# Optimization experiments

Measured on AMD Instinct MI355X. Metric: run time of the kernel, lower is better.

Reference implementation:

```python
import jax, jax.numpy as jnp
import numpy as np

EMBED_DIM = 512
NUM_HEADS = 8
HEAD_DIM = EMBED_DIM // NUM_HEADS


def setup_inputs() -> dict:
    key = jax.random.key(0)
    ks = jax.random.split(key, 9)
    s = 1.0 / np.sqrt(EMBED_DIM)
    x = jax.random.normal(ks[0], (2, 4096, EMBED_DIM), dtype=jnp.float32)
    return {
        "x": x,
        "Wq": jax.random.uniform(ks[1], (EMBED_DIM, EMBED_DIM), jnp.float32, -s, s),
        "bq": jax.random.uniform(ks[2], (EMBED_DIM,), jnp.float32, -s, s),
        "Wk": jax.random.uniform(ks[3], (EMBED_DIM, EMBED_DIM), jnp.float32, -s, s),
        "bk": jax.random.uniform(ks[4], (EMBED_DIM,), jnp.float32, -s, s),
        "Wv": jax.random.uniform(ks[5], (EMBED_DIM, EMBED_DIM), jnp.float32, -s, s),
        "bv": jax.random.uniform(ks[6], (EMBED_DIM,), jnp.float32, -s, s),
        "Wo": jax.random.uniform(ks[7], (EMBED_DIM, EMBED_DIM), jnp.float32, -s, s),
        "bo": jax.random.uniform(ks[8], (EMBED_DIM,), jnp.float32, -s, s),
    }


def reference(x, Wq, bq, Wk, bk, Wv, bv, Wo, bo):
    B, S, E = x.shape
    H, D = NUM_HEADS, HEAD_DIM
    # projections (torch Linear: x @ W.T + b)
    q = (x @ Wq.T + bq).reshape(B, S, H, D).transpose(0, 2, 1, 3)  # [B,H,S,D]
    k = (x @ Wk.T + bk).reshape(B, S, H, D).transpose(0, 2, 1, 3)
    v = (x @ Wv.T + bv).reshape(B, S, H, D).transpose(0, 2, 1, 3)
    scores = jnp.einsum("bhsd,bhtd->bhst", q, k) / np.sqrt(D)  # [B,H,S,S]
    attn = jax.nn.softmax(scores, axis=-1)
    out = jnp.einsum("bhst,bhtd->bhsd", attn, v)  # [B,H,S,D]
    out = out.transpose(0, 2, 1, 3).reshape(B, S, E)
    return out @ Wo.T + bo + x
```

## Files before the change

kernel.cpp:

```cpp
#include <hip/hip_runtime.h>
#include <hip/hip_bf16.h>


typedef __attribute__((ext_vector_type(8))) short short8;
typedef __attribute__((ext_vector_type(4))) short short4v;
typedef __attribute__((ext_vector_type(4))) float floatx4;
typedef __attribute__((ext_vector_type(2))) float floatx2;

#define SEQ 4096
#define EMB 512
#define NH 8
#define HD 64
#define MROWS 8192
#define SC2 0.18033688011112042f

__device__ inline unsigned short f2bf_rne(float f) {
    union { float f; unsigned int u; } c; c.f = f;
    unsigned int u = c.u;
    return (unsigned short)((u + 0x7FFFu + ((u >> 16) & 1u)) >> 16);
}

__device__ inline short8 load8f(const float* __restrict__ p) {
    float4 a = *(const float4*)p;
    float4 b = *(const float4*)(p + 4);
    short8 r;
    r[0] = (short)f2bf_rne(a.x); r[1] = (short)f2bf_rne(a.y);
    r[2] = (short)f2bf_rne(a.z); r[3] = (short)f2bf_rne(a.w);
    r[4] = (short)f2bf_rne(b.x); r[5] = (short)f2bf_rne(b.y);
    r[6] = (short)f2bf_rne(b.z); r[7] = (short)f2bf_rne(b.w);
    return r;
}

__device__ inline void gload_lds16(const unsigned short* g, unsigned short* l) {
    __builtin_amdgcn_global_load_lds(
        (__attribute__((address_space(1))) void*)(void*)g,
        (__attribute__((address_space(3))) void*)l,
        16, 0, 0);
}

__device__ inline unsigned int pk_bf2(float a, float b) {
    union { float f; unsigned int u; } ca, cb; ca.f = a; cb.f = b;
    return __builtin_amdgcn_perm(cb.u + 0x8000u, ca.u + 0x8000u, 0x07060302u);
}

__device__ inline unsigned int pk_bf2t(float a, float b) {
    union { float f; unsigned int u; } ca, cb; ca.f = a; cb.f = b;
    return __builtin_amdgcn_perm(cb.u, ca.u, 0x07060302u);
}

__global__ __launch_bounds__(256) void convert_kernel(
    const float* __restrict__ x, const float* __restrict__ Wq,
    const float* __restrict__ Wk, const float* __restrict__ Wv,
    const float* __restrict__ Wo, unsigned short* __restrict__ xb,
    unsigned short* __restrict__ wb)
{
    const size_t i8 = ((size_t)blockIdx.x * 256 + threadIdx.x) * 8;
    const float* src; unsigned short* dst;
    if (i8 < (size_t)MROWS * EMB) { src = x + i8; dst = xb + i8; }
    else {
        size_t j = i8 - (size_t)MROWS * EMB;
        int w = (int)(j >> 18); size_t off = j & 262143;
        src = (w == 0 ? Wq : w == 1 ? Wk : w == 2 ? Wv : Wo) + off;
        dst = wb + (size_t)w * 262144 + off;
    }
    *(short8*)dst = load8f(src);
}

__global__ __launch_bounds__(256) void qkv_kernel(
    const unsigned short* __restrict__ xb, const unsigned short* __restrict__ wb,
    const float* __restrict__ bq, const float* __restrict__ bk,
    const float* __restrict__ bv, unsigned short* __restrict__ Qo,
    unsigned short* __restrict__ Ko, unsigned short* __restrict__ VTo)
{
    __shared__ unsigned short smem[32768];

    const int tid = threadIdx.x, wave = tid >> 6, lane = tid & 63;
    const int quad = lane >> 4, l16 = lane & 15;
    const int wm = wave >> 1, wn = wave & 1;
    const int row0 = blockIdx.x * 128, col0 = blockIdx.y * 128;
    const int z = blockIdx.z;

    unsigned short* sA = smem;
    unsigned short* sB = smem + 16384;

    const unsigned short* A = xb + (size_t)row0 * EMB;
    const unsigned short* Bm = wb + (size_t)z * 262144 + (size_t)col0 * EMB;
    const float* bias = z == 0 ? bq : z == 1 ? bk : bv;
    unsigned short* out = z == 0 ? Qo : z == 1 ? Ko : VTo;

    auto stage = [&](int buf, int k0) {
#pragma unroll
        for (int it = 0; it < 4; ++it) {
            const int s = it * 256 + tid;
            const int row = s >> 3, cg = (s & 7) ^ (row & 7);
            const size_t go = (size_t)row * EMB + k0 + cg * 8;
            gload_lds16(A + go, &sA[buf * 8192 + (it * 256 + wave * 64) * 8]);
            gload_lds16(Bm + go, &sB[buf * 8192 + (it * 256 + wave * 64) * 8]);
        }
    };

    floatx4 acc[4][4];
#pragma unroll
    for (int i = 0; i < 4; ++i)
#pragma unroll
        for (int j = 0; j < 4; ++j) { floatx4 zz = {0.f,0.f,0.f,0.f}; acc[i][j] = zz; }

    stage(0, 0);
    int buf = 0;
    for (int k0 = 0; k0 < EMB; k0 += 64) {
        __syncthreads();
        if (k0 + 64 < EMB) stage(buf ^ 1, k0 + 64);
#pragma unroll
        for (int kk = 0; kk < 2; ++kk) {
            short8 a[4], b[4];
#pragma unroll
            for (int mi = 0; mi < 4; ++mi)
                a[mi] = *(const short8*)&sA[buf * 8192 + (wm * 64 + mi * 16 + l16) * 64 + (((kk * 4 + quad) ^ (l16 & 7)) << 3)];
#pragma unroll
            for (int ni = 0; ni < 4; ++ni)
                b[ni] = *(const short8*)&sB[buf * 8192 + (wn * 64 + ni * 16 + l16) * 64 + (((kk * 4 + quad) ^ (l16 & 7)) << 3)];
            if (z != 2) {
#pragma unroll
                for (int i = 0; i < 4; ++i)
#pragma unroll
                    for (int j = 0; j < 4; ++j)
                        acc[i][j] = __builtin_amdgcn_mfma_f32_16x16x32_bf16(b[i], a[j], acc[i][j], 0, 0, 0);
            } else {
#pragma unroll
                for (int i = 0; i < 4; ++i)
#pragma unroll
                    for (int j = 0; j < 4; ++j)
                        acc[i][j] = __builtin_amdgcn_mfma_f32_16x16x32_bf16(a[i], b[j], acc[i][j], 0, 0, 0);
            }
        }
        buf ^= 1;
    }

    __syncthreads();
    unsigned short* ct = smem;
    const float qs = (z == 0) ? SC2 : 1.0f;
    if (z != 2) {
#pragma unroll
        for (int i = 0; i < 4; ++i) {
            const int n0 = wn * 64 + i * 16 + quad * 4;
            const float4 fb = *(const float4*)&bias[col0 + n0];
#pragma unroll
            for (int j = 0; j < 4; ++j) {
                const int m = wm * 64 + j * 16 + l16;
                ushort4 pk;
                pk.x = f2bf_rne((acc[i][j][0] + fb.x) * qs);
                pk.y = f2bf_rne((acc[i][j][1] + fb.y) * qs);
                pk.z = f2bf_rne((acc[i][j][2] + fb.z) * qs);
                pk.w = f2bf_rne((acc[i][j][3] + fb.w) * qs);
                *(ushort4*)&ct[m * 132 + n0] = pk;
            }
        }
    } else {
#pragma unroll
        for (int j = 0; j < 4; ++j) {
            const int n = wn * 64 + j * 16 + l16;
            const float fb = bias[col0 + n];
#pragma unroll
            for (int i = 0; i < 4; ++i) {
                const int m0 = wm * 64 + i * 16 + quad * 4;
                ushort4 pk;
                pk.x = f2bf_rne(acc[i][j][0] + fb);
                pk.y = f2bf_rne(acc[i][j][1] + fb);
                pk.z = f2bf_rne(acc[i][j][2] + fb);
                pk.w = f2bf_rne(acc[i][j][3] + fb);
                *(ushort4*)&ct[n * 132 + m0] = pk;
            }
        }
    }
    __syncthreads();
#pragma unroll
    for (int it = 0; it < 8; ++it) {
        const int idx = it * 256 + tid;
        const int row = idx >> 4, chunk = idx & 15;
        short8 v = *(const short8*)&ct[row * 132 + chunk * 8];
        size_t addr;
        if (z != 2) {
            const int m_g = row0 + row;
            const int b = m_g >> 12, s = m_g & 4095;
            const int n_g = col0 + chunk * 8;
            const int h = n_g >> 6, d = n_g & 63;
            addr = ((size_t)((b * NH + h) * SEQ + s)) * HD + d;
        } else {
            const int n_g = col0 + row;
            const int h = n_g >> 6, d = n_g & 63;
            const int m_g = row0 + chunk * 8;
            const int b = m_g >> 12, s0 = m_g & 4095;
            addr = ((size_t)((b * NH + h) * HD + d)) * SEQ + s0;
        }
        *(short8*)&out[addr] = v;
    }
}

__global__ __launch_bounds__(512) void attn_kernel(
    const unsigned short* __restrict__ Q, const unsigned short* __restrict__ K,
    const unsigned short* __restrict__ VT, unsigned short* __restrict__ Oout)
{
    __shared__ unsigned short sK[2][2][4096];
    __shared__ unsigned short sVT[2][2][4096];

    const int tid = threadIdx.x, wave = tid >> 6, lane = tid & 63;
    const int quad = lane >> 4, l16 = lane & 15;
    const int bh = blockIdx.x, q0 = blockIdx.y * 128;
    const int xm = l16 & 7;

    const unsigned short* Qh = Q + (size_t)bh * SEQ * HD;
    const unsigned short* Kh = K + (size_t)bh * SEQ * HD;
    const unsigned short* Vh = VT + (size_t)bh * HD * SEQ;

    short8 qf[2];
#pragma unroll
    for (int kk = 0; kk < 2; ++kk)
        qf[kk] = *(const short8*)(Qh + (size_t)(q0 + wave * 16 + l16) * HD + kk * 32 + quad * 8);

    int kbase[4], kx0[4], kx1[4];
#pragma unroll
    for (int nt = 0; nt < 4; ++nt) {
        const int g = nt >> 1, T = nt & 1;
        const int R = g * 32 + ((l16 >> 2) << 3) + (T << 2) + (l16 & 3);
        const int fR = (R & 7) ^ ((R >> 2) & 7);
        kbase[nt] = R * 64;
        kx0[nt] = (quad ^ fR) << 3;
        kx1[nt] = ((4 + quad) ^ fR) << 3;
    }

    floatx4 oacc[4];
#pragma unroll
    for (int dt = 0; dt < 4; ++dt) { floatx4 zz = {0.f,0.f,0.f,0.f}; oacc[dt] = zz; }
    floatx2 psum2 = {0.f, 0.f};
    const floatx4 z4 = {0.f, 0.f, 0.f, 0.f};

    auto stage = [&](int buf, int t0) {
        const int r = tid >> 3, j = tid & 7;
        const int cK = j ^ ((r & 7) ^ ((r >> 2) & 7));
        const int cV = j ^ (r & 7);
#pragma unroll
        for (int sub = 0; sub < 2; ++sub) {
            gload_lds16(Kh + (size_t)(t0 + sub * 64 + r) * HD + cK * 8, &sK[buf][sub][wave * 512]);
            gload_lds16(Vh + (size_t)r * SEQ + t0 + sub * 64 + cV * 8, &sVT[buf][sub][wave * 512]);
        }
    };

    stage(0, 0);
    int buf = 0;
    for (int t0 = 0; t0 < SEQ; t0 += 128) {
        __syncthreads();
        if (t0 + 128 < SEQ) stage(buf ^ 1, t0 + 128);

#pragma unroll
        for (int sub = 0; sub < 2; ++sub) {
            const unsigned short* sKs  = sK[buf][sub];
            const unsigned short* sVTs = sVT[buf][sub];

            floatx4 stf[4];
            {
                short8 bK[4];
#pragma unroll
                for (int nt = 0; nt < 4; ++nt)
                    bK[nt] = *(const short8*)&sKs[kbase[nt] + kx0[nt]];
#pragma unroll
                for (int nt = 0; nt < 4; ++nt)
                    stf[nt] = __builtin_amdgcn_mfma_f32_16x16x32_bf16(bK[nt], qf[0], z4, 0, 0, 0);
            }
            {
                short8 bK[4];
#pragma unroll
                for (int nt = 0; nt < 4; ++nt)
                    bK[nt] = *(const short8*)&sKs[kbase[nt] + kx1[nt]];
#pragma unroll
                for (int nt = 0; nt < 4; ++nt)
                    stf[nt] = __builtin_amdgcn_mfma_f32_16x16x32_bf16(bK[nt], qf[1], stf[nt], 0, 0, 0);
            }

            short8 paf[2];
#pragma unroll
            for (int g = 0; g < 2; ++g) {
                float e[8];
#pragma unroll
                for (int T = 0; T < 2; ++T)
#pragma unroll
                    for (int r = 0; r < 4; ++r)
                        e[T * 4 + r] = __builtin_amdgcn_exp2f(stf[g * 2 + T][r]);
                floatx2 pa = {e[0], e[1]}, pb = {e[2], e[3]};
                floatx2 pc = {e[4], e[5]}, pd = {e[6], e[7]};
                psum2 += (pa + pb) + (pc + pd);
                union { uint4 u; short8 s; } cv;
                cv.u.x = pk_bf2t(e[0], e[1]);
                cv.u.y = pk_bf2t(e[2], e[3]);
                cv.u.z = pk_bf2t(e[4], e[5]);
                cv.u.w = pk_bf2t(e[6], e[7]);
                paf[g] = cv.s;
            }

#pragma unroll
            for (int g = 0; g < 2; ++g) {
                short8 bv8[4];
#pragma unroll
                for (int dt = 0; dt < 4; ++dt)
                    bv8[dt] = *(const short8*)&sVTs[(dt * 16 + l16) * 64 + (((g * 4 + quad) ^ xm) << 3)];
#pragma unroll
                for (int dt = 0; dt < 4; ++dt)
                    oacc[dt] = __builtin_amdgcn_mfma_f32_16x16x32_bf16(paf[g], bv8[dt], oacc[dt], 0, 0, 0);
            }
        }
        buf ^= 1;
    }

    float psum = psum2[0] + psum2[1];
    psum += __shfl_xor(psum, 16);
    psum += __shfl_xor(psum, 32);

    const int b = bh >> 3, h = bh & 7;
#pragma unroll
    for (int r = 0; r < 4; ++r) {
        const float inv = 1.0f / __shfl(psum, quad * 4 + r);
        const int s = q0 + wave * 16 + quad * 4 + r;
        const size_t base = ((size_t)b * SEQ + s) * EMB + h * HD;
#pragma unroll
        for (int dt = 0; dt < 4; ++dt)
            Oout[base + dt * 16 + l16] = f2bf_rne(oacc[dt][r] * inv);
    }
}

__global__ __launch_bounds__(256) void outproj_kernel(
    const unsigned short* __restrict__ Ain, const unsigned short* __restrict__ wob,
    const float* __restrict__ bias, const float* __restrict__ X,
    float* __restrict__ out)
{
    __shared__ unsigned short sA[2][4096];
    __shared__ unsigned short sB[2][8192];

    const int tid = threadIdx.x, wave = tid >> 6, lane = tid & 63;
    const int quad = lane >> 4, l16 = lane & 15;
    const int wm = wave >> 1, wn = wave & 1;
    const int row0 = blockIdx.x * 64, col0 = blockIdx.y * 128;

    const unsigned short* A = Ain + (size_t)row0 * EMB;
    const unsigned short* Bm = wob + (size_t)col0 * EMB;

    auto stage = [&](int buf, int k0) {
#pragma unroll
        for (int it = 0; it < 2; ++it) {
            const int s = it * 256 + tid;
            const int row = s >> 3, cg = (s & 7) ^ (row & 7);
            gload_lds16(A + (size_t)row * EMB + k0 + cg * 8, &sA[buf][(it * 256 + wave * 64) * 8]);
        }
#pragma unroll
        for (int it = 0; it < 4; ++it) {
            const int s = it * 256 + tid;
            const int row = s >> 3, cg = (s & 7) ^ (row & 7);
            gload_lds16(Bm + (size_t)row * EMB + k0 + cg * 8, &sB[buf][(it * 256 + wave * 64) * 8]);
        }
    };

    floatx4 acc[2][4];
#pragma unroll
    for (int mi = 0; mi < 2; ++mi)
#pragma unroll
        for (int ni = 0; ni < 4; ++ni) { floatx4 zz = {0.f,0.f,0.f,0.f}; acc[mi][ni] = zz; }

    stage(0, 0);
    int buf = 0;
    for (int k0 = 0; k0 < EMB; k0 += 64) {
        __syncthreads();
        if (k0 + 64 < EMB) stage(buf ^ 1, k0 + 64);
#pragma unroll
        for (int kk = 0; kk < 2; ++kk) {
            short8 a[2], b[4];
#pragma unroll
            for (int mi = 0; mi < 2; ++mi)
                a[mi] = *(const short8*)&sA[buf][(wm * 32 + mi * 16 + l16) * 64 + (((kk * 4 + quad) ^ (l16 & 7)) << 3)];
#pragma unroll
            for (int ni = 0; ni < 4; ++ni)
                b[ni] = *(const short8*)&sB[buf][(wn * 64 + ni * 16 + l16) * 64 + (((kk * 4 + quad) ^ (l16 & 7)) << 3)];
#pragma unroll
            for (int mi = 0; mi < 2; ++mi)
#pragma unroll
                for (int ni = 0; ni < 4; ++ni)
                    acc[mi][ni] = __builtin_amdgcn_mfma_f32_16x16x32_bf16(a[mi], b[ni], acc[mi][ni], 0, 0, 0);
        }
        buf ^= 1;
    }

#pragma unroll
    for (int mi = 0; mi < 2; ++mi)
#pragma unroll
        for (int ni = 0; ni < 4; ++ni) {
            const int n = col0 + wn * 64 + ni * 16 + l16;
            const float bs = bias[n];
#pragma unroll
            for (int r = 0; r < 4; ++r) {
                const int m = row0 + wm * 32 + mi * 16 + quad * 4 + r;
                const size_t idx = (size_t)m * EMB + n;
                out[idx] = acc[mi][ni][r] + bs + X[idx];
            }
        }
}

extern "C" void kernel_launch(void* const* d_in, const int* in_sizes, int n_in,
                              void* d_out, int out_size, void* d_ws, size_t ws_size,
                              hipStream_t stream) {
    const float* x  = (const float*)d_in[0];
    const float* Wq = (const float*)d_in[1];
    const float* bq = (const float*)d_in[2];
    const float* Wk = (const float*)d_in[3];
    const float* bk = (const float*)d_in[4];
    const float* Wv = (const float*)d_in[5];
    const float* bv = (const float*)d_in[6];
    const float* Wo = (const float*)d_in[7];
    const float* bo = (const float*)d_in[8];
    float* out = (float*)d_out;

    const size_t SZ = (size_t)MROWS * EMB;
    unsigned short* wsXB = (unsigned short*)d_ws;
    unsigned short* wsWB = wsXB + SZ;
    unsigned short* wsQ  = wsWB + 4 * 262144;
    unsigned short* wsK  = wsQ + SZ;
    unsigned short* wsVT = wsK + SZ;

    convert_kernel<<<2560, 256, 0, stream>>>(x, Wq, Wk, Wv, Wo, wsXB, wsWB);
    qkv_kernel<<<dim3(MROWS / 128, EMB / 128, 3), 256, 0, stream>>>(
        wsXB, wsWB, bq, bk, bv, wsQ, wsK, wsVT);
    attn_kernel<<<dim3(2 * NH, SEQ / 128), 512, 0, stream>>>(wsQ, wsK, wsVT, wsXB);
    outproj_kernel<<<dim3(MROWS / 64, EMB / 128), 256, 0, stream>>>(
        wsXB, wsWB + 3 * 262144, bo, x, out);
}
```

Measured before the change: 192.4 us.

## Split attention key dimension across waves with cross-wave output reduction

Reworks the attention kernel so each 256-thread block handles 64 queries and each wave owns a 32-key slice of every 128-key tile while covering all 64 query rows. Partial P·V outputs are then reduced across waves through shared memory. The row sums of exp are now computed with an MFMA against a ones vector instead of VALU adds. This is meant to reuse K/V fragments loaded from LDS across four query sub-tiles and to allow two blocks per CU, at the cost of more accumulator registers and an extra shared-memory reduction at the end.

New measurement: 198.2 us. +3.0%, slower.

```diff
diff --git a/kernel.cpp b/kernel.cpp
--- a/kernel.cpp
+++ b/kernel.cpp
@@ -196,52 +196,63 @@
     }
 }
 
-__global__ __launch_bounds__(512) void attn_kernel(
+__global__ __launch_bounds__(256, 2) void attn_kernel(
     const unsigned short* __restrict__ Q, const unsigned short* __restrict__ K,
     const unsigned short* __restrict__ VT, unsigned short* __restrict__ Oout)
 {
-    __shared__ unsigned short sK[2][2][4096];
-    __shared__ unsigned short sVT[2][2][4096];
+    __shared__ unsigned short smem[32768];
+    __shared__ float sPS[256];
 
     const int tid = threadIdx.x, wave = tid >> 6, lane = tid & 63;
     const int quad = lane >> 4, l16 = lane & 15;
-    const int bh = blockIdx.x, q0 = blockIdx.y * 128;
+    const int bh = blockIdx.x, q0 = blockIdx.y * 64;
     const int xm = l16 & 7;
 
     const unsigned short* Qh = Q + (size_t)bh * SEQ * HD;
     const unsigned short* Kh = K + (size_t)bh * SEQ * HD;
     const unsigned short* Vh = VT + (size_t)bh * HD * SEQ;
 
-    short8 qf[2];
-#pragma unroll
-    for (int kk = 0; kk < 2; ++kk)
-        qf[kk] = *(const short8*)(Qh + (size_t)(q0 + wave * 16 + l16) * HD + kk * 32 + quad * 8);
-
-    int kbase[4], kx0[4], kx1[4];
-#pragma unroll
-    for (int nt = 0; nt < 4; ++nt) {
-        const int g = nt >> 1, T = nt & 1;
-        const int R = g * 32 + ((l16 >> 2) << 3) + (T << 2) + (l16 & 3);
+    short8 qf[4][2];
+#pragma unroll
+    for (int mi = 0; mi < 4; ++mi)
+#pragma unroll
+        for (int kk = 0; kk < 2; ++kk)
+            qf[mi][kk] = *(const short8*)(Qh + (size_t)(q0 + mi * 16 + l16) * HD + kk * 32 + quad * 8);
+
+    int kbase[2], kx0[2], kx1[2];
+#pragma unroll
+    for (int T = 0; T < 2; ++T) {
+        const int R = wave * 32 + ((l16 >> 2) << 3) + (T << 2) + (l16 & 3);
         const int fR = (R & 7) ^ ((R >> 2) & 7);
-        kbase[nt] = R * 64;
-        kx0[nt] = (quad ^ fR) << 3;
-        kx1[nt] = ((4 + quad) ^ fR) << 3;
-    }
-
-    floatx4 oacc[4];
-#pragma unroll
-    for (int dt = 0; dt < 4; ++dt) { floatx4 zz = {0.f,0.f,0.f,0.f}; oacc[dt] = zz; }
-    floatx2 psum2 = {0.f, 0.f};
+        kbase[T] = R * 64;
+        kx0[T] = (quad ^ fR) << 3;
+        kx1[T] = ((4 + quad) ^ fR) << 3;
+    }
+
+    floatx4 oacc[4][4];
+#pragma unroll
+    for (int mi = 0; mi < 4; ++mi)
+#pragma unroll
+        for (int dt = 0; dt < 4; ++dt) { floatx4 zz = {0.f,0.f,0.f,0.f}; oacc[mi][dt] = zz; }
+    floatx4 sacc[4];
+#pragma unroll
+    for (int mi = 0; mi < 4; ++mi) { floatx4 zz = {0.f,0.f,0.f,0.f}; sacc[mi] = zz; }
     const floatx4 z4 = {0.f, 0.f, 0.f, 0.f};
+    const short ob = (short)0x3F80;
+    const short8 ones8 = {ob, ob, ob, ob, ob, ob, ob, ob};
 
     auto stage = [&](int buf, int t0) {
-        const int r = tid >> 3, j = tid & 7;
-        const int cK = j ^ ((r & 7) ^ ((r >> 2) & 7));
-        const int cV = j ^ (r & 7);
-#pragma unroll
-        for (int sub = 0; sub < 2; ++sub) {
-            gload_lds16(Kh + (size_t)(t0 + sub * 64 + r) * HD + cK * 8, &sK[buf][sub][wave * 512]);
-            gload_lds16(Vh + (size_t)r * SEQ + t0 + sub * 64 + cV * 8, &sVT[buf][sub][wave * 512]);
+        unsigned short* sK  = &smem[buf * 16384];
+        unsigned short* sVT = &smem[buf * 16384 + 8192];
+#pragma unroll
+        for (int it = 0; it < 4; ++it) {
+            const int s = it * 256 + tid;
+            const int rK = s >> 3, jK = s & 7;
+            const int cK = jK ^ ((rK & 7) ^ ((rK >> 2) & 7));
+            gload_lds16(Kh + (size_t)(t0 + rK) * HD + cK * 8, &sK[(it * 256 + wave * 64) * 8]);
+            const int rV = s >> 4, jV = s & 15;
+            const int cV = jV ^ (rV & 7);
+            gload_lds16(Vh + (size_t)rV * SEQ + t0 + cV * 8, &sVT[(it * 256 + wave * 64) * 8]);
         }
     };
 
@@ -251,78 +262,93 @@
         __syncthreads();
         if (t0 + 128 < SEQ) stage(buf ^ 1, t0 + 128);
 
-#pragma unroll
-        for (int sub = 0; sub < 2; ++sub) {
-            const unsigned short* sKs  = sK[buf][sub];
-            const unsigned short* sVTs = sVT[buf][sub];
-
-            floatx4 stf[4];
-            {
-                short8 bK[4];
-#pragma unroll
-                for (int nt = 0; nt < 4; ++nt)
-                    bK[nt] = *(const short8*)&sKs[kbase[nt] + kx0[nt]];
-#pragma unroll
-                for (int nt = 0; nt < 4; ++nt)
-                    stf[nt] = __builtin_amdgcn_mfma_f32_16x16x32_bf16(bK[nt], qf[0], z4, 0, 0, 0);
+        const unsigned short* sKs  = &smem[buf * 16384];
+        const unsigned short* sVTs = &smem[buf * 16384 + 8192];
+
+        short8 bK0[2], bK1[2];
+#pragma unroll
+        for (int T = 0; T < 2; ++T) {
+            bK0[T] = *(const short8*)&sKs[kbase[T] + kx0[T]];
+            bK1[T] = *(const short8*)&sKs[kbase[T] + kx1[T]];
+        }
+        short8 bv8[4];
+#pragma unroll
+        for (int dt = 0; dt < 4; ++dt)
+            bv8[dt] = *(const short8*)&sVTs[(dt * 16 + l16) * 128 + (((wave * 4 + quad) ^ xm) << 3)];
+
+#pragma unroll
+        for (int mi = 0; mi < 4; ++mi) {
+            floatx4 s0 = __builtin_amdgcn_mfma_f32_16x16x32_bf16(bK0[0], qf[mi][0], z4, 0, 0, 0);
+            floatx4 s1 = __builtin_amdgcn_mfma_f32_16x16x32_bf16(bK0[1], qf[mi][0], z4, 0, 0, 0);
+            s0 = __builtin_amdgcn_mfma_f32_16x16x32_bf16(bK1[0], qf[mi][1], s0, 0, 0, 0);
+            s1 = __builtin_amdgcn_mfma_f32_16x16x32_bf16(bK1[1], qf[mi][1], s1, 0, 0, 0);
+
+            float e0 = __builtin_amdgcn_exp2f(s0[0]);
+            float e1 = __builtin_amdgcn_exp2f(s0[1]);
+            float e2 = __builtin_amdgcn_exp2f(s0[2]);
+            float e3 = __builtin_amdgcn_exp2f(s0[3]);
+            float e4 = __builtin_amdgcn_exp2f(s1[0]);
+            float e5 = __builtin_amdgcn_exp2f(s1[1]);
+            float e6 = __builtin_amdgcn_exp2f(s1[2]);
+            float e7 = __builtin_amdgcn_exp2f(s1[3]);
+            union { uint4 u; short8 s; } cv;
+            cv.u.x = pk_bf2t(e0, e1);
+            cv.u.y = pk_bf2t(e2, e3);
+            cv.u.z = pk_bf2t(e4, e5);
+            cv.u.w = pk_bf2t(e6, e7);
+            const short8 paf = cv.s;
+
+            sacc[mi] = __builtin_amdgcn_mfma_f32_16x16x32_bf16(paf, ones8, sacc[mi], 0, 0, 0);
+#pragma unroll
+            for (int dt = 0; dt < 4; ++dt)
+                oacc[mi][dt] = __builtin_amdgcn_mfma_f32_16x16x32_bf16(paf, bv8[dt], oacc[mi][dt], 0, 0, 0);
+        }
+        buf ^= 1;
+    }
+
+    if (l16 == 0) {
+#pragma unroll
+        for (int mi = 0; mi < 4; ++mi)
+#pragma unroll
+            for (int r = 0; r < 4; ++r)
+                sPS[wave * 64 + mi * 16 + quad * 4 + r] = sacc[mi][r];
+    }
+
+    float* sRed = (float*)smem;
+    const int b = bh >> 3, h = bh & 7;
+    const int qr = wave * 16 + l16;
+
+#pragma unroll
+    for (int hh = 0; hh < 2; ++hh) {
+        __syncthreads();
+#pragma unroll
+        for (int mi = 0; mi < 4; ++mi)
+#pragma unroll
+            for (int dd = 0; dd < 2; ++dd)
+#pragma unroll
+                for (int r = 0; r < 4; ++r)
+                    sRed[wave * 2176 + (mi * 16 + quad * 4 + r) * 34 + dd * 16 + l16] =
+                        oacc[mi][hh * 2 + dd][r];
+        __syncthreads();
+        floatx2 o8[4] = {{0.f,0.f},{0.f,0.f},{0.f,0.f},{0.f,0.f}};
+#pragma unroll
+        for (int w2 = 0; w2 < 4; ++w2) {
+            const float* base = &sRed[w2 * 2176 + qr * 34 + quad * 8];
+#pragma unroll
+            for (int p = 0; p < 4; ++p) {
+                floatx2 v = *(const floatx2*)(base + p * 2);
+                o8[p] += v;
             }
-            {
-                short8 bK[4];
-#pragma unroll
-                for (int nt = 0; nt < 4; ++nt)
-                    bK[nt] = *(const short8*)&sKs[kbase[nt] + kx1[nt]];
-#pragma unroll
-                for (int nt = 0; nt < 4; ++nt)
-                    stf[nt] = __builtin_amdgcn_mfma_f32_16x16x32_bf16(bK[nt], qf[1], stf[nt], 0, 0, 0);
-            }
-
-            short8 paf[2];
-#pragma unroll
-            for (int g = 0; g < 2; ++g) {
-                float e[8];
-#pragma unroll
-                for (int T = 0; T < 2; ++T)
-#pragma unroll
-                    for (int r = 0; r < 4; ++r)
-                        e[T * 4 + r] = __builtin_amdgcn_exp2f(stf[g * 2 + T][r]);
-                floatx2 pa = {e[0], e[1]}, pb = {e[2], e[3]};
-                floatx2 pc = {e[4], e[5]}, pd = {e[6], e[7]};
-                psum2 += (pa + pb) + (pc + pd);
-                union { uint4 u; short8 s; } cv;
-                cv.u.x = pk_bf2t(e[0], e[1]);
-                cv.u.y = pk_bf2t(e[2], e[3]);
-                cv.u.z = pk_bf2t(e[4], e[5]);
-                cv.u.w = pk_bf2t(e[6], e[7]);
-                paf[g] = cv.s;
-            }
-
-#pragma unroll
-            for (int g = 0; g < 2; ++g) {
-                short8 bv8[4];
-#pragma unroll
-                for (int dt = 0; dt < 4; ++dt)
-                    bv8[dt] = *(const short8*)&sVTs[(dt * 16 + l16) * 64 + (((g * 4 + quad) ^ xm) << 3)];
-#pragma unroll
-                for (int dt = 0; dt < 4; ++dt)
-                    oacc[dt] = __builtin_amdgcn_mfma_f32_16x16x32_bf16(paf[g], bv8[dt], oacc[dt], 0, 0, 0);
-            }
-        }
-        buf ^= 1;
-    }
-
-    float psum = psum2[0] + psum2[1];
-    psum += __shfl_xor(psum, 16);
-    psum += __shfl_xor(psum, 32);
-
-    const int b = bh >> 3, h = bh & 7;
-#pragma unroll
-    for (int r = 0; r < 4; ++r) {
-        const float inv = 1.0f / __shfl(psum, quad * 4 + r);
-        const int s = q0 + wave * 16 + quad * 4 + r;
-        const size_t base = ((size_t)b * SEQ + s) * EMB + h * HD;
-#pragma unroll
-        for (int dt = 0; dt < 4; ++dt)
-            Oout[base + dt * 16 + l16] = f2bf_rne(oacc[dt][r] * inv);
+        }
+        const float pst = sPS[qr] + sPS[64 + qr] + sPS[128 + qr] + sPS[192 + qr];
+        const float inv = 1.0f / pst;
+        union { uint4 u; short8 s; } pk;
+        pk.u.x = pk_bf2(o8[0][0] * inv, o8[0][1] * inv);
+        pk.u.y = pk_bf2(o8[1][0] * inv, o8[1][1] * inv);
+        pk.u.z = pk_bf2(o8[2][0] * inv, o8[2][1] * inv);
+        pk.u.w = pk_bf2(o8[3][0] * inv, o8[3][1] * inv);
+        const size_t addr = ((size_t)b * SEQ + q0 + qr) * EMB + h * HD + hh * 32 + quad * 8;
+        *(short8*)&Oout[addr] = pk.s;
     }
 }
 
@@ -425,7 +451,7 @@
     convert_kernel<<<2560, 256, 0, stream>>>(x, Wq, Wk, Wv, Wo, wsXB, wsWB);
     qkv_kernel<<<dim3(MROWS / 128, EMB / 128, 3), 256, 0, stream>>>(
         wsXB, wsWB, bq, bk, bv, wsQ, wsK, wsVT);
-    attn_kernel<<<dim3(2 * NH, SEQ / 128), 512, 0, stream>>>(wsQ, wsK, wsVT, wsXB);
+    attn_kernel<<<dim3(2 * NH, SEQ / 64), 256, 0, stream>>>(wsQ, wsK, wsVT, wsXB);
     outproj_kernel<<<dim3(MROWS / 64, EMB / 128), 256, 0, stream>>>(
         wsXB, wsWB + 3 * 262144, bo, x, out);
 }
```
